# Optimization experiments

Hardware: AMD Instinct MI355X
Metric: run time of the kernel (lower is better)

Reference implementation:

```python
import jax, jax.numpy as jnp
import numpy as np

C, A, K, S = 128, 64, 24, 4           # molecules, atoms, neighbors, species
RCR, RCA = 5.2, 3.5                   # radial / angular cutoffs (Angstrom)
ETA_R, ETA_A, ZETA = 16.0, 8.0, 32.0
LAYERS = [384, 160, 128, 96, 1]       # per-element MLP
NPAIR = S * (S + 1) // 2              # 10 unordered species pairs

_triu = np.zeros((S, S), np.int32)
_c = 0
for _i in range(S):
    for _j in range(_i, S):
        _triu[_i, _j] = _triu[_j, _i] = _c
        _c += 1
TRIU = jnp.asarray(_triu)
JJ, KK = np.triu_indices(K, 1)        # static pair-of-neighbors indices, T = K(K-1)/2


def setup_inputs() -> dict:
    key = jax.random.key(0)
    ks = jax.random.split(key, 12)
    element_idxs = jax.random.randint(ks[0], (C, A), 0, S, dtype=jnp.int32)
    neighbor_idxs = jax.random.randint(ks[1], (C, A, K), 0, A, dtype=jnp.int32)
    distances = jax.random.uniform(ks[2], (C, A, K), minval=0.8, maxval=5.0, dtype=jnp.float32)
    dirs = jax.random.normal(ks[3], (C, A, K, 3), dtype=jnp.float32)
    dirs = dirs / jnp.linalg.norm(dirs, axis=-1, keepdims=True)
    diff_vectors = dirs * distances[..., None]
    inp = {"element_idxs": element_idxs, "neighbor_idxs": neighbor_idxs,
           "distances": distances, "diff_vectors": diff_vectors}
    k = 4
    for i, (fin, fout) in enumerate(zip(LAYERS[:-1], LAYERS[1:]), 1):
        inp[f"W{i}"] = jax.random.normal(ks[k], (S, fin, fout), dtype=jnp.float32) / np.sqrt(fin).astype(np.float32); k += 1
        inp[f"b{i}"] = jax.random.normal(ks[k], (S, fout), dtype=jnp.float32) * 0.01; k += 1
    return inp


def _fc(d, rc):
    # smooth cosine cutoff, exactly zero beyond rc
    return jnp.where(d < rc, 0.5 * jnp.cos(np.float32(np.pi) * d / rc) + 0.5, 0.0)


def _celu(x, a=0.1):
    return jnp.where(x > 0, x, a * jnp.expm1(x / a))


def reference(element_idxs, neighbor_idxs, distances, diff_vectors,
              W1, b1, W2, b2, W3, b3, W4, b4):
    shfr = jnp.linspace(0.9, RCR, 17, dtype=jnp.float32)[:-1]                 # (16,)
    shfa = jnp.linspace(0.9, RCA, 5, dtype=jnp.float32)[:-1]                  # (4,)
    shfz = (jnp.arange(8, dtype=jnp.float32) + 0.5) * np.float32(np.pi / 8)   # (8,)

    # species of each neighbor: (C,A,K)
    nspec = element_idxs[jnp.arange(C)[:, None, None], neighbor_idxs]

    # ---- radial sub-AEV: (C,A,S,16) ----
    fcr = _fc(distances, RCR)
    rterm = 0.25 * jnp.exp(-ETA_R * (distances[..., None] - shfr) ** 2) * fcr[..., None]  # (C,A,K,16)
    oh_s = jax.nn.one_hot(nspec, S, dtype=rterm.dtype)                                     # (C,A,K,S)
    radial = jnp.einsum('cakr,caks->casr', rterm, oh_s).reshape(C, A, S * 16)

    # ---- angular sub-AEV over neighbor pairs (j<k): T = K(K-1)/2 ----
    d1, d2 = distances[..., JJ], distances[..., KK]                 # (C,A,T)
    v1, v2 = diff_vectors[..., JJ, :], diff_vectors[..., KK, :]      # (C,A,T,3)
    cosang = jnp.sum(v1 * v2, axis=-1) / (d1 * d2)
    ang = jnp.arccos(0.95 * cosang)                                  # torchani's 0.95 nan-guard
    f1 = ((1.0 + jnp.cos(ang[..., None] - shfz)) * 0.5) ** ZETA      # (C,A,T,8)
    f2 = jnp.exp(-ETA_A * ((d1 + d2) * 0.5)[..., None] - shfa * 0.0) if False else \
         jnp.exp(-ETA_A * (((d1 + d2) * 0.5)[..., None] - shfa) ** 2)  # (C,A,T,4)
    fc12 = _fc(d1, RCA) * _fc(d2, RCA)                               # (C,A,T)
    aterm = (2.0 * f1[..., :, None] * f2[..., None, :] * fc12[..., None, None]).reshape(C, A, JJ.size, 32)
    pidx = TRIU[nspec[..., JJ], nspec[..., KK]]                      # (C,A,T) in [0,10)
    oh_p = jax.nn.one_hot(pidx, NPAIR, dtype=aterm.dtype)            # (C,A,T,10)
    angular = jnp.einsum('catf,catp->capf', aterm, oh_p).reshape(C, A, NPAIR * 32)

    aev = jnp.concatenate([radial, angular], axis=-1)                # (C,A,384)

    # ---- per-element MLPs (computed for all species, then gathered) ----
    h = _celu(jnp.einsum('caf,sfo->caso', aev, W1) + b1)
    h = _celu(jnp.einsum('casf,sfo->caso', h, W2) + b2)
    h = _celu(jnp.einsum('casf,sfo->caso', h, W3) + b3)
    out = (jnp.einsum('casf,sfo->caso', h, W4) + b4)[..., 0]         # (C,A,S)
    atomic = jnp.take_along_axis(out, element_idxs[..., None], axis=2)[..., 0]  # (C,A)
    return atomic.sum(axis=-1)                                       # (C,) molecular energies
```

## Files before the change

### kernel.cpp

```cpp
#include <hip/hip_runtime.h>
#include <math.h>

constexpr int C_ = 128, A_ = 64, K_ = 24, S_ = 4;
constexpr int NATOM = C_ * A_;
constexpr int FAEV = 384;
constexpr float RCR = 5.2f, RCA = 3.5f;
constexpr float PI_F = 3.14159265358979323846f;
constexpr float K_A2 = -8.0f  * 1.44269504f;
constexpr float K_R2 = -64.0f * 1.44269504f;
constexpr float SQRT095 = 0.974679434f;
constexpr float SQRT2   = 1.41421356237f;

__global__ __launch_bounds__(1024) void setup_kernel(const int* __restrict__ elem,
                                                     int* __restrict__ cnt,
                                                     int* __restrict__ glist,
                                                     float* __restrict__ out) {
    __shared__ int cnt_s[S_];
    const int t = threadIdx.x;
    const int lane = t & 63;
    if (t < S_) cnt_s[t] = 0;
    if (t < C_) out[t] = 0.0f;
    __syncthreads();
    for (int a = t; a < NATOM; a += 1024) {
        int sp = elem[a];
        unsigned long long lt = (lane == 0) ? 0ULL : ((~0ULL) >> (64 - lane));
        int pos = 0;
        #pragma unroll
        for (int q = 0; q < S_; ++q) {
            unsigned long long m = __ballot(sp == q);
            int cw = (int)__popcll(m);
            int b = 0;
            if (lane == 0 && cw) b = atomicAdd(&cnt_s[q], cw);
            b = __shfl(b, 0);
            if (sp == q) pos = b + (int)__popcll(m & lt);
        }
        glist[sp * NATOM + pos] = a;
    }
    __syncthreads();
    if (t < S_) cnt[t] = cnt_s[t];
}

__global__ __launch_bounds__(512, 4) void fused_kernel(const int* __restrict__ elem,
                                                       const int* __restrict__ nbr,
                                                       const float* __restrict__ dist,
                                                       const float* __restrict__ dv,
                                                       const int* __restrict__ cnt,
                                                       const int* __restrict__ glist,
                                                       const float* __restrict__ W1, const float* __restrict__ b1,
                                                       const float* __restrict__ W2, const float* __restrict__ b2,
                                                       const float* __restrict__ W3, const float* __restrict__ b3,
                                                       const float* __restrict__ W4, const float* __restrict__ b4,
                                                       float* __restrict__ out) {
    const int s     = blockIdx.x >> 8;
    const int tile0 = blockIdx.x & 255;
    const int t     = threadIdx.x;
    const int w     = t >> 6;
    const int lane  = t & 63;
    const int cntS  = cnt[s];

    __shared__ float4        u4_s[8][K_];
    __shared__ float         fcr_s[8][K_];
    __shared__ float         fca_s[8][K_];
    __shared__ int           spec_s[8][K_];
    __shared__ unsigned char bidx_s[8][S_][K_];
    __shared__ int           atom_sh[8];
    __shared__ __attribute__((aligned(16))) float aev_s[8][FAEV];
    __shared__ __attribute__((aligned(16))) float h1_s[8][160];
    float (*h2_s)[128] = (float(*)[128])&aev_s[0][0];
    float (*h3_s)[96]  = (float(*)[96])(&aev_s[0][0] + 8 * 128);

    const float* W1s = W1 + s * (FAEV * 160);
    const float* b1s = b1 + s * 160;
    const float* W2s = W2 + s * (160 * 128);
    const float* b2s = b2 + s * 128;
    const float* W3s = W3 + s * (128 * 96);
    const float* b3s = b3 + s * 96;
    const float* W4s = W4 + s * 96;
    const float  bb4 = b4[s];

    const int lane32 = lane & 31;
    const int par    = lane >> 5;
    const int zz = lane32 >> 2, yy = lane32 & 3;
    const float cz2 = 0.5f * __cosf(((float)zz + 0.5f) * (PI_F / 8.0f));
    const float sz2 = 0.5f * __sinf(((float)zz + 0.5f) * (PI_F / 8.0f));
    const float shfa_l = 0.9f + 0.65f * (float)yy;
    const unsigned long long ltmask = (lane == 0) ? 0ULL : ((~0ULL) >> (64 - lane));

    for (int tile = tile0; tile * 8 < cntS; tile += 256) {
        const int g = tile * 8 + w;
        const int atomAbs = (g < cntS) ? glist[s * NATOM + g] : -1;
        if (lane == 0) atom_sh[w] = atomAbs;

        int   mySpec = -1;
        float myFca  = 0.0f;
        if (atomAbs >= 0 && lane < K_) {
            int base = atomAbs * K_ + lane;
            int c    = atomAbs >> 6;
            int nb   = nbr[base];
            float d  = dist[base];
            float inv = __builtin_amdgcn_rcpf(d) * SQRT095;
            float4 u;
            u.x = dv[base * 3 + 0] * inv;
            u.y = dv[base * 3 + 1] * inv;
            u.z = dv[base * 3 + 2] * inv;
            u.w = 0.5f * d;
            u4_s[w][lane]  = u;
            mySpec = elem[(c << 6) + nb];
            spec_s[w][lane] = mySpec;
            fcr_s[w][lane] = (d < RCR) ? (0.5f * __cosf(PI_F * d * (1.0f / RCR)) + 0.5f) : 0.0f;
            myFca = (d < RCA) ? (SQRT2 * (0.5f * __cosf(PI_F * d * (1.0f / RCA)) + 0.5f)) : 0.0f;
            fca_s[w][lane] = myFca;
        }

        int nspR[S_];
        {
            const bool act = (myFca > 0.0f);
            #pragma unroll
            for (int q = 0; q < S_; ++q) {
                unsigned long long mk = __ballot(act && (mySpec == q));
                if (act && (mySpec == q))
                    bidx_s[w][q][(int)__popcll(mk & ltmask)] = (unsigned char)lane;
                nspR[q] = (int)__popcll(mk);
            }
        }

        if (atomAbs >= 0) {
            {
                const int   spg   = lane >> 4;
                const float shfrh = 0.5f * (0.9f + 0.26875f * (float)(lane & 15));
                float acc = 0.0f;
                #pragma unroll
                for (int k = 0; k < K_; ++k) {
                    float hd = u4_s[w][k].w;
                    float df = hd - shfrh;
                    float term = 0.25f * exp2f(df * df * K_R2) * fcr_s[w][k];
                    if (spec_s[w][k] == spg) acc += term;
                }
                aev_s[w][lane] = acc;
            }
            auto pair_term = [&](int j, int k2) -> float {
                float4 u1 = u4_s[w][j], u2 = u4_s[w][k2];
                float ca = u1.x * u2.x + u1.y * u2.y + u1.z * u2.z;
                float sa = __builtin_amdgcn_sqrtf(1.0f - ca * ca);
                float dd = (u1.w + u2.w) - shfa_l;
                float f2 = exp2f(dd * dd * K_A2);
                float x  = 0.5f + ca * cz2 + sa * sz2;
                float x2 = x * x, x4 = x2 * x2, x8 = x4 * x4, x16 = x8 * x8;
                float tc = fca_s[w][j] * fca_s[w][k2];
                return (x16 * x16) * (f2 * tc);
            };
            #pragma unroll
            for (int spa = 0; spa < 4; ++spa) {
                #pragma unroll
                for (int spb = spa; spb < 4; ++spb) {
                    const int pidx = spa * (9 - spa) / 2 + (spb - spa);
                    const int na = nspR[spa];
                    float acc = 0.0f;
                    if (spa == spb) {
                        const int   T   = (na * (na - 1)) >> 1;
                        const float ff  = (float)(2 * na - 1);
                        const float ff2 = ff * ff;
                        for (int q = par; q < T; q += 2) {
                            float sq = __builtin_amdgcn_sqrtf(ff2 - 8.0f * (float)q);
                            int i = (int)((ff - sq) * 0.5f);
                            int st1 = (i + 1) * (na - 1) - (((i + 1) * i) >> 1);
                            if (st1 <= q) ++i;
                            int st = i * (na - 1) - ((i * (i - 1)) >> 1);
                            if (st > q) { --i; st = i * (na - 1) - ((i * (i - 1)) >> 1); }
                            int j2 = q - st + i + 1;
                            acc += pair_term((int)bidx_s[w][spa][i], (int)bidx_s[w][spa][j2]);
                        }
                    } else {
                        const int   nb2 = nspR[spb];
                        const int   T   = na * nb2;
                        const float rcp = __builtin_amdgcn_rcpf((float)nb2);
                        for (int q = par; q < T; q += 2) {
                            int i  = (int)(((float)q + 0.5f) * rcp);
                            int j2 = q - i * nb2;
                            acc += pair_term((int)bidx_s[w][spa][i], (int)bidx_s[w][spb][j2]);
                        }
                    }
                    float other = __shfl(acc, lane32 + 32);
                    if (lane < 32) aev_s[w][64 + pidx * 32 + lane32] = acc + other;
                }
            }
        }
        __syncthreads();

        if (t < 320) {
            const int h  = (t >= 160) ? 1 : 0;
            const int o  = t - h * 160;
            const int mb = h * 4;
            const float* Wp = W1s + o;
            float acc[4] = {0.f, 0.f, 0.f, 0.f};
            float wa[4], wb[4];
            #pragma unroll
            for (int j = 0; j < 4; ++j) wa[j] = Wp[j * 160];
            for (int f = 0; f < FAEV; f += 8) {
                const int fb = f + 4;
                #pragma unroll
                for (int j = 0; j < 4; ++j) wb[j] = Wp[(fb + j) * 160];
                #pragma unroll
                for (int m = 0; m < 4; ++m) {
                    float4 av = *(const float4*)&aev_s[mb + m][f];
                    acc[m] += av.x * wa[0] + av.y * wa[1] + av.z * wa[2] + av.w * wa[3];
                }
                const int fa = (f + 8 < FAEV) ? f + 8 : 0;
                #pragma unroll
                for (int j = 0; j < 4; ++j) wa[j] = Wp[(fa + j) * 160];
                #pragma unroll
                for (int m = 0; m < 4; ++m) {
                    float4 av = *(const float4*)&aev_s[mb + m][fb];
                    acc[m] += av.x * wb[0] + av.y * wb[1] + av.z * wb[2] + av.w * wb[3];
                }
            }
            float bb = b1s[o];
            #pragma unroll
            for (int m = 0; m < 4; ++m) {
                float x = acc[m] + bb;
                h1_s[mb + m][o] = (x > 0.f) ? x : 0.1f * (__expf(10.f * x) - 1.f);
            }
        }
        __syncthreads();

        if (t < 256) {
            const int h  = t >> 7;
            const int o  = t & 127;
            const int mb = h * 4;
            const float* Wp = W2s + o;
            float acc[4] = {0.f, 0.f, 0.f, 0.f};
            float wa[4], wb[4];
            #pragma unroll
            for (int j = 0; j < 4; ++j) wa[j] = Wp[j * 128];
            for (int f = 0; f < 160; f += 8) {
                const int fb = f + 4;
                #pragma unroll
                for (int j = 0; j < 4; ++j) wb[j] = Wp[(fb + j) * 128];
                #pragma unroll
                for (int m = 0; m < 4; ++m) {
                    float4 av = *(const float4*)&h1_s[mb + m][f];
                    acc[m] += av.x * wa[0] + av.y * wa[1] + av.z * wa[2] + av.w * wa[3];
                }
                const int fa = (f + 8 < 160) ? f + 8 : 0;
                #pragma unroll
                for (int j = 0; j < 4; ++j) wa[j] = Wp[(fa + j) * 128];
                #pragma unroll
                for (int m = 0; m < 4; ++m) {
                    float4 av = *(const float4*)&h1_s[mb + m][fb];
                    acc[m] += av.x * wb[0] + av.y * wb[1] + av.z * wb[2] + av.w * wb[3];
                }
            }
            float bb = b2s[o];
            #pragma unroll
            for (int m = 0; m < 4; ++m) {
                float x = acc[m] + bb;
                h2_s[mb + m][o] = (x > 0.f) ? x : 0.1f * (__expf(10.f * x) - 1.f);
            }
        }
        __syncthreads();

        if (t < 192) {
            const int h  = (t >= 96) ? 1 : 0;
            const int o  = t - h * 96;
            const int mb = h * 4;
            const float* Wp = W3s + o;
            float acc[4] = {0.f, 0.f, 0.f, 0.f};
            float wa[4], wb[4];
            #pragma unroll
            for (int j = 0; j < 4; ++j) wa[j] = Wp[j * 96];
            for (int f = 0; f < 128; f += 8) {
                const int fb = f + 4;
                #pragma unroll
                for (int j = 0; j < 4; ++j) wb[j] = Wp[(fb + j) * 96];
                #pragma unroll
                for (int m = 0; m < 4; ++m) {
                    float4 av = *(const float4*)&h2_s[mb + m][f];
                    acc[m] += av.x * wa[0] + av.y * wa[1] + av.z * wa[2] + av.w * wa[3];
                }
                const int fa = (f + 8 < 128) ? f + 8 : 0;
                #pragma unroll
                for (int j = 0; j < 4; ++j) wa[j] = Wp[(fa + j) * 96];
                #pragma unroll
                for (int m = 0; m < 4; ++m) {
                    float4 av = *(const float4*)&h2_s[mb + m][fb];
                    acc[m] += av.x * wb[0] + av.y * wb[1] + av.z * wb[2] + av.w * wb[3];
                }
            }
            float bb = b3s[o];
            #pragma unroll
            for (int m = 0; m < 4; ++m) {
                float x = acc[m] + bb;
                h3_s[mb + m][o] = (x > 0.f) ? x : 0.1f * (__expf(10.f * x) - 1.f);
            }
        }
        __syncthreads();

        if (t < 256) {
            int m = t >> 5, l = t & 31;
            int a = atom_sh[m];
            if (a >= 0) {
                float p = h3_s[m][l]      * W4s[l]
                        + h3_s[m][l + 32] * W4s[l + 32]
                        + h3_s[m][l + 64] * W4s[l + 64];
                #pragma unroll
                for (int off = 16; off >= 1; off >>= 1)
                    p += __shfl_xor(p, off, 32);
                if (l == 0) atomicAdd(&out[a >> 6], p + bb4);
            }
        }
        __syncthreads();
    }
}

extern "C" void kernel_launch(void* const* d_in, const int* in_sizes, int n_in,
                              void* d_out, int out_size, void* d_ws, size_t ws_size,
                              hipStream_t stream) {
    const int*   element_idxs  = (const int*)d_in[0];
    const int*   neighbor_idxs = (const int*)d_in[1];
    const float* distances     = (const float*)d_in[2];
    const float* diff_vectors  = (const float*)d_in[3];
    const float* W1 = (const float*)d_in[4];
    const float* b1 = (const float*)d_in[5];
    const float* W2 = (const float*)d_in[6];
    const float* b2 = (const float*)d_in[7];
    const float* W3 = (const float*)d_in[8];
    const float* b3 = (const float*)d_in[9];
    const float* W4 = (const float*)d_in[10];
    const float* b4 = (const float*)d_in[11];
    float* out = (float*)d_out;

    int* cnt   = (int*)d_ws;
    int* glist = cnt + 4;

    hipLaunchKernelGGL(setup_kernel, dim3(1), dim3(1024), 0, stream,
                       element_idxs, cnt, glist, out);
    hipLaunchKernelGGL(fused_kernel, dim3(S_ * 256), dim3(512), 0, stream,
                       element_idxs, neighbor_idxs, distances, diff_vectors,
                       cnt, glist,
                       W1, b1, W2, b2, W3, b3, W4, b4, out);
}
```

Measured before the change: 231.9 us.

## Halve block to four atoms and replace triangular index math with nested loops

Each block now handles four atoms with 256 threads instead of eight atoms with 512, and the grid doubles to 2048 blocks. The MLP layers drop the two-half split, so each thread computes one output column for four atoms. The angular pair enumeration replaces the sqrt-based decoding of a flat triangular index with explicit nested i/j loops, and the outer neighbor's vector and cutoff are hoisted out of the inner loop. This cuts per-pair index arithmetic and gives finer-grained blocks, but weights are now reloaded per four atoms rather than per eight, and parity-split inner loops may leave lanes unevenly loaded.

After: 235.1 us. About the same (+1.4%).

```diff
diff --git a/kernel.cpp b/kernel.cpp
--- a/kernel.cpp
+++ b/kernel.cpp
@@ -40,7 +40,7 @@
     if (t < S_) cnt[t] = cnt_s[t];
 }
 
-__global__ __launch_bounds__(512, 4) void fused_kernel(const int* __restrict__ elem,
+__global__ __launch_bounds__(256, 4) void fused_kernel(const int* __restrict__ elem,
                                                        const int* __restrict__ nbr,
                                                        const float* __restrict__ dist,
                                                        const float* __restrict__ dv,
@@ -51,23 +51,23 @@
                                                        const float* __restrict__ W3, const float* __restrict__ b3,
                                                        const float* __restrict__ W4, const float* __restrict__ b4,
                                                        float* __restrict__ out) {
-    const int s     = blockIdx.x >> 8;
-    const int tile0 = blockIdx.x & 255;
+    const int s     = blockIdx.x >> 9;
+    const int tile0 = blockIdx.x & 511;
     const int t     = threadIdx.x;
     const int w     = t >> 6;
     const int lane  = t & 63;
     const int cntS  = cnt[s];
 
-    __shared__ float4        u4_s[8][K_];
-    __shared__ float         fcr_s[8][K_];
-    __shared__ float         fca_s[8][K_];
-    __shared__ int           spec_s[8][K_];
-    __shared__ unsigned char bidx_s[8][S_][K_];
-    __shared__ int           atom_sh[8];
-    __shared__ __attribute__((aligned(16))) float aev_s[8][FAEV];
-    __shared__ __attribute__((aligned(16))) float h1_s[8][160];
+    __shared__ float4        u4_s[4][K_];
+    __shared__ float         fcr_s[4][K_];
+    __shared__ float         fca_s[4][K_];
+    __shared__ int           spec_s[4][K_];
+    __shared__ unsigned char bidx_s[4][S_][K_];
+    __shared__ int           atom_sh[4];
+    __shared__ __attribute__((aligned(16))) float aev_s[4][FAEV];
+    __shared__ __attribute__((aligned(16))) float h1_s[4][160];
     float (*h2_s)[128] = (float(*)[128])&aev_s[0][0];
-    float (*h3_s)[96]  = (float(*)[96])(&aev_s[0][0] + 8 * 128);
+    float (*h3_s)[96]  = (float(*)[96])(&aev_s[0][0] + 4 * 128);
 
     const float* W1s = W1 + s * (FAEV * 160);
     const float* b1s = b1 + s * 160;
@@ -86,8 +86,8 @@
     const float shfa_l = 0.9f + 0.65f * (float)yy;
     const unsigned long long ltmask = (lane == 0) ? 0ULL : ((~0ULL) >> (64 - lane));
 
-    for (int tile = tile0; tile * 8 < cntS; tile += 256) {
-        const int g = tile * 8 + w;
+    for (int tile = tile0; tile * 4 < cntS; tile += 512) {
+        const int g = tile * 4 + w;
         const int atomAbs = (g < cntS) ? glist[s * NATOM + g] : -1;
         if (lane == 0) atom_sh[w] = atomAbs;
 
@@ -138,15 +138,15 @@
                 }
                 aev_s[w][lane] = acc;
             }
-            auto pair_term = [&](int j, int k2) -> float {
-                float4 u1 = u4_s[w][j], u2 = u4_s[w][k2];
+            auto pair_term = [&](const float4& u1, float fca1, int k2) -> float {
+                float4 u2 = u4_s[w][k2];
                 float ca = u1.x * u2.x + u1.y * u2.y + u1.z * u2.z;
                 float sa = __builtin_amdgcn_sqrtf(1.0f - ca * ca);
                 float dd = (u1.w + u2.w) - shfa_l;
                 float f2 = exp2f(dd * dd * K_A2);
                 float x  = 0.5f + ca * cz2 + sa * sz2;
                 float x2 = x * x, x4 = x2 * x2, x8 = x4 * x4, x16 = x8 * x8;
-                float tc = fca_s[w][j] * fca_s[w][k2];
+                float tc = fca1 * fca_s[w][k2];
                 return (x16 * x16) * (f2 * tc);
             };
             #pragma unroll
@@ -154,30 +154,24 @@
                 #pragma unroll
                 for (int spb = spa; spb < 4; ++spb) {
                     const int pidx = spa * (9 - spa) / 2 + (spb - spa);
-                    const int na = nspR[spa];
+                    const int na  = nspR[spa];
+                    const int nb2 = nspR[spb];
                     float acc = 0.0f;
                     if (spa == spb) {
-                        const int   T   = (na * (na - 1)) >> 1;
-                        const float ff  = (float)(2 * na - 1);
-                        const float ff2 = ff * ff;
-                        for (int q = par; q < T; q += 2) {
-                            float sq = __builtin_amdgcn_sqrtf(ff2 - 8.0f * (float)q);
-                            int i = (int)((ff - sq) * 0.5f);
-                            int st1 = (i + 1) * (na - 1) - (((i + 1) * i) >> 1);
-                            if (st1 <= q) ++i;
-                            int st = i * (na - 1) - ((i * (i - 1)) >> 1);
-                            if (st > q) { --i; st = i * (na - 1) - ((i * (i - 1)) >> 1); }
-                            int j2 = q - st + i + 1;
-                            acc += pair_term((int)bidx_s[w][spa][i], (int)bidx_s[w][spa][j2]);
+                        for (int i = 0; i < na - 1; ++i) {
+                            int ji = (int)bidx_s[w][spa][i];
+                            float4 u1 = u4_s[w][ji];
+                            float fca1 = fca_s[w][ji];
+                            for (int j = i + 1 + par; j < na; j += 2)
+                                acc += pair_term(u1, fca1, (int)bidx_s[w][spa][j]);
                         }
                     } else {
-                        const int   nb2 = nspR[spb];
-                        const int   T   = na * nb2;
-                        const float rcp = __builtin_amdgcn_rcpf((float)nb2);
-                        for (int q = par; q < T; q += 2) {
-                            int i  = (int)(((float)q + 0.5f) * rcp);
-                            int j2 = q - i * nb2;
-                            acc += pair_term((int)bidx_s[w][spa][i], (int)bidx_s[w][spb][j2]);
+                        for (int i = 0; i < na; ++i) {
+                            int ji = (int)bidx_s[w][spa][i];
+                            float4 u1 = u4_s[w][ji];
+                            float fca1 = fca_s[w][ji];
+                            for (int j = par; j < nb2; j += 2)
+                                acc += pair_term(u1, fca1, (int)bidx_s[w][spb][j]);
                         }
                     }
                     float other = __shfl(acc, lane32 + 32);
@@ -187,11 +181,8 @@
         }
         __syncthreads();
 
-        if (t < 320) {
-            const int h  = (t >= 160) ? 1 : 0;
-            const int o  = t - h * 160;
-            const int mb = h * 4;
-            const float* Wp = W1s + o;
+        if (t < 160) {
+            const float* Wp = W1s + t;
             float acc[4] = {0.f, 0.f, 0.f, 0.f};
             float wa[4], wb[4];
             #pragma unroll
@@ -202,7 +193,7 @@
                 for (int j = 0; j < 4; ++j) wb[j] = Wp[(fb + j) * 160];
                 #pragma unroll
                 for (int m = 0; m < 4; ++m) {
-                    float4 av = *(const float4*)&aev_s[mb + m][f];
+                    float4 av = *(const float4*)&aev_s[m][f];
                     acc[m] += av.x * wa[0] + av.y * wa[1] + av.z * wa[2] + av.w * wa[3];
                 }
                 const int fa = (f + 8 < FAEV) ? f + 8 : 0;
@@ -210,24 +201,21 @@
                 for (int j = 0; j < 4; ++j) wa[j] = Wp[(fa + j) * 160];
                 #pragma unroll
                 for (int m = 0; m < 4; ++m) {
-                    float4 av = *(const float4*)&aev_s[mb + m][fb];
+                    float4 av = *(const float4*)&aev_s[m][fb];
                     acc[m] += av.x * wb[0] + av.y * wb[1] + av.z * wb[2] + av.w * wb[3];
                 }
             }
-            float bb = b1s[o];
+            float bb = b1s[t];
             #pragma unroll
             for (int m = 0; m < 4; ++m) {
                 float x = acc[m] + bb;
-                h1_s[mb + m][o] = (x > 0.f) ? x : 0.1f * (__expf(10.f * x) - 1.f);
-            }
-        }
-        __syncthreads();
-
-        if (t < 256) {
-            const int h  = t >> 7;
-            const int o  = t & 127;
-            const int mb = h * 4;
-            const float* Wp = W2s + o;
+                h1_s[m][t] = (x > 0.f) ? x : 0.1f * (__expf(10.f * x) - 1.f);
+            }
+        }
+        __syncthreads();
+
+        if (t < 128) {
+            const float* Wp = W2s + t;
             float acc[4] = {0.f, 0.f, 0.f, 0.f};
             float wa[4], wb[4];
             #pragma unroll
@@ -238,7 +226,7 @@
                 for (int j = 0; j < 4; ++j) wb[j] = Wp[(fb + j) * 128];
                 #pragma unroll
                 for (int m = 0; m < 4; ++m) {
-                    float4 av = *(const float4*)&h1_s[mb + m][f];
+                    float4 av = *(const float4*)&h1_s[m][f];
                     acc[m] += av.x * wa[0] + av.y * wa[1] + av.z * wa[2] + av.w * wa[3];
                 }
                 const int fa = (f + 8 < 160) ? f + 8 : 0;
@@ -246,24 +234,21 @@
                 for (int j = 0; j < 4; ++j) wa[j] = Wp[(fa + j) * 128];
                 #pragma unroll
                 for (int m = 0; m < 4; ++m) {
-                    float4 av = *(const float4*)&h1_s[mb + m][fb];
+                    float4 av = *(const float4*)&h1_s[m][fb];
                     acc[m] += av.x * wb[0] + av.y * wb[1] + av.z * wb[2] + av.w * wb[3];
                 }
             }
-            float bb = b2s[o];
+            float bb = b2s[t];
             #pragma unroll
             for (int m = 0; m < 4; ++m) {
                 float x = acc[m] + bb;
-                h2_s[mb + m][o] = (x > 0.f) ? x : 0.1f * (__expf(10.f * x) - 1.f);
-            }
-        }
-        __syncthreads();
-
-        if (t < 192) {
-            const int h  = (t >= 96) ? 1 : 0;
-            const int o  = t - h * 96;
-            const int mb = h * 4;
-            const float* Wp = W3s + o;
+                h2_s[m][t] = (x > 0.f) ? x : 0.1f * (__expf(10.f * x) - 1.f);
+            }
+        }
+        __syncthreads();
+
+        if (t < 96) {
+            const float* Wp = W3s + t;
             float acc[4] = {0.f, 0.f, 0.f, 0.f};
             float wa[4], wb[4];
             #pragma unroll
@@ -274,7 +259,7 @@
                 for (int j = 0; j < 4; ++j) wb[j] = Wp[(fb + j) * 96];
                 #pragma unroll
                 for (int m = 0; m < 4; ++m) {
-                    float4 av = *(const float4*)&h2_s[mb + m][f];
+                    float4 av = *(const float4*)&h2_s[m][f];
                     acc[m] += av.x * wa[0] + av.y * wa[1] + av.z * wa[2] + av.w * wa[3];
                 }
                 const int fa = (f + 8 < 128) ? f + 8 : 0;
@@ -282,20 +267,20 @@
                 for (int j = 0; j < 4; ++j) wa[j] = Wp[(fa + j) * 96];
                 #pragma unroll
                 for (int m = 0; m < 4; ++m) {
-                    float4 av = *(const float4*)&h2_s[mb + m][fb];
+                    float4 av = *(const float4*)&h2_s[m][fb];
                     acc[m] += av.x * wb[0] + av.y * wb[1] + av.z * wb[2] + av.w * wb[3];
                 }
             }
-            float bb = b3s[o];
+            float bb = b3s[t];
             #pragma unroll
             for (int m = 0; m < 4; ++m) {
                 float x = acc[m] + bb;
-                h3_s[mb + m][o] = (x > 0.f) ? x : 0.1f * (__expf(10.f * x) - 1.f);
-            }
-        }
-        __syncthreads();
-
-        if (t < 256) {
+                h3_s[m][t] = (x > 0.f) ? x : 0.1f * (__expf(10.f * x) - 1.f);
+            }
+        }
+        __syncthreads();
+
+        if (t < 128) {
             int m = t >> 5, l = t & 31;
             int a = atom_sh[m];
             if (a >= 0) {
@@ -334,7 +319,7 @@
 
     hipLaunchKernelGGL(setup_kernel, dim3(1), dim3(1024), 0, stream,
                        element_idxs, cnt, glist, out);
-    hipLaunchKernelGGL(fused_kernel, dim3(S_ * 256), dim3(512), 0, stream,
+    hipLaunchKernelGGL(fused_kernel, dim3(S_ * 512), dim3(256), 0, stream,
                        element_idxs, neighbor_idxs, distances, diff_vectors,
                        cnt, glist,
                        W1, b1, W2, b2, W3, b3, W4, b4, out);
```
